# Kernel optimization log

Measured on AMD Instinct MI355X. Metric: run time of the kernel, lower is better.

The kernel has to match this reference:

```python
import jax, jax.numpy as jnp
import numpy as np

B, S, D, H = 2, 2048, 1024, 16
DH = D // H  # 64


def setup_inputs() -> dict:
    key = jax.random.key(0)
    ks = jax.random.split(key, 10)
    inp = {
        "q": jax.random.normal(ks[0], (B, S, D), jnp.float32),
        "k": jax.random.normal(ks[1], (B, S, D), jnp.float32),
        "v": jax.random.normal(ks[2], (B, S, D), jnp.float32),
        "mask": jax.random.randint(ks[3], (B, S), 0, 2, jnp.int32),
        "Wq": jax.random.normal(ks[4], (D, D), jnp.float32) * 0.02,
        "bq": jnp.zeros((D,), jnp.float32),
        "Wk": jax.random.normal(ks[5], (D, D), jnp.float32) * 0.02,
        "bk": jnp.zeros((D,), jnp.float32),
        "Wv": jax.random.normal(ks[6], (D, D), jnp.float32) * 0.02,
        "bv": jnp.zeros((D,), jnp.float32),
    }
    return inp


def _split_heads(x):
    # [B, S, D] -> [B, H, S, DH]
    b, s, _ = x.shape
    return x.reshape(b, s, H, DH).transpose(0, 2, 1, 3)


def reference(q, k, v, mask, Wq, bq, Wk, bk, Wv, bv):
    qh = _split_heads(q @ Wq + bq)
    kh = _split_heads(k @ Wk + bk)
    vh = _split_heads(v @ Wv + bv)
    # NOTE: original scales by sqrt(hidden_size), not sqrt(head_dim)
    scores = jnp.einsum("bhqd,bhkd->bhqk", qh, kh) / jnp.sqrt(jnp.float32(D))
    m = mask.astype(jnp.float32)[:, None, None, :]  # [B,1,1,S_k]
    scores = scores + (-1e9) * (1.0 - m)
    weights = jax.nn.softmax(scores, axis=-1)
    out = jnp.einsum("bhqk,bhkd->bhqd", weights, vh)
    # concat heads: [B,H,S,DH] -> [B,S,D]
    return out.transpose(0, 2, 1, 3).reshape(q.shape[0], -1, D)
```

## Files before the change

### kernel.cpp

```cpp
#include <hip/hip_runtime.h>


#define B_ 2
#define S_ 2048
#define D_ 1024
#define H_ 16
#define DH_ 64
#define M_ (B_*S_)

#define WT_OFF  ((size_t)3*4194304)
#define XB_OFF  (WT_OFF + (size_t)3*1048576)

typedef __attribute__((ext_vector_type(8))) short short8;
typedef __attribute__((ext_vector_type(4))) float f32x4;
#define MFMA16(a,b,c) __builtin_amdgcn_mfma_f32_16x16x32_bf16(a,b,c,0,0,0)

typedef __attribute__((address_space(1))) const void* gptr_t;
typedef __attribute__((address_space(3))) void* lptr_t;
static __device__ inline void gload_lds16(const void* g, void* l) {
    __builtin_amdgcn_global_load_lds((gptr_t)g, (lptr_t)l, 16, 0, 0);
}

static __device__ inline unsigned short f2bf(float x) {
    union { float f; unsigned u; } v; v.f = x;
    return (unsigned short)((v.u + 0x7fffu + ((v.u >> 16) & 1u)) >> 16);
}
static __device__ inline unsigned packp(float a, float b) {
    return __builtin_amdgcn_perm(__float_as_uint(b) + 0x8000u,
                                 __float_as_uint(a) + 0x8000u, 0x07060302u);
}

__global__ __launch_bounds__(256) void convert_x3(
    const float* __restrict__ X0, const float* __restrict__ X1,
    const float* __restrict__ X2, unsigned short* __restrict__ O0,
    unsigned short* __restrict__ O1, unsigned short* __restrict__ O2)
{
    const int z = blockIdx.z;
    const float* X = z==0 ? X0 : (z==1 ? X1 : X2);
    unsigned short* O = z==0 ? O0 : (z==1 ? O1 : O2);
    int idx = blockIdx.x*256 + threadIdx.x;
    float4 xv = *(const float4*)&X[(size_t)idx*4];
    uint2 o;
    o.x = (unsigned)f2bf(xv.x) | ((unsigned)f2bf(xv.y) << 16);
    o.y = (unsigned)f2bf(xv.z) | ((unsigned)f2bf(xv.w) << 16);
    *(uint2*)&O[(size_t)idx*4] = o;
}

__global__ __launch_bounds__(256) void convert_w(
    const float* __restrict__ Wq, const float* __restrict__ Wk,
    const float* __restrict__ Wv, unsigned short* __restrict__ WtBase)
{
    const int which = blockIdx.z;
    const float* W = which==0 ? Wq : (which==1 ? Wk : Wv);
    unsigned short* Out = WtBase + ((size_t)which << 20);

    __shared__ unsigned short T[64][72];
    const int t  = threadIdx.x;
    const int n0 = blockIdx.x*64, k0 = blockIdx.y*64;
    const int tk = t >> 4, tn4 = (t & 15)*4;

    #pragma unroll
    for (int i=0;i<4;i++){
        int kk = tk + i*16;
        float4 wv = *(const float4*)&W[(size_t)(k0+kk)*D_ + n0 + tn4];
        T[tn4+0][kk] = f2bf(wv.x);
        T[tn4+1][kk] = f2bf(wv.y);
        T[tn4+2][kk] = f2bf(wv.z);
        T[tn4+3][kk] = f2bf(wv.w);
    }
    __syncthreads();

    const int n = t >> 2, seg = t & 3;
    uint4 a = *(uint4*)&T[n][seg*16];
    uint4 b = *(uint4*)&T[n][seg*16 + 8];
    *(uint4*)&Out[(size_t)(n0+n)*D_ + k0 + seg*16]     = a;
    *(uint4*)&Out[(size_t)(n0+n)*D_ + k0 + seg*16 + 8] = b;
}

__global__ __launch_bounds__(256) void proj_gemm(
    const unsigned short* __restrict__ A0, const unsigned short* __restrict__ A1,
    const unsigned short* __restrict__ A2, const unsigned short* __restrict__ WtBase,
    const float* __restrict__ b0, const float* __restrict__ b1,
    const float* __restrict__ b2, unsigned short* __restrict__ OutBase)
{
    const int which = blockIdx.z;
    const unsigned short* A  = which==0 ? A0 : (which==1 ? A1 : A2);
    const unsigned short* Bm = WtBase + ((size_t)which << 20);
    const float* bias        = which==0 ? b0 : (which==1 ? b1 : b2);
    unsigned short* Out      = OutBase + ((size_t)which << 22);
    const float oscale = (which==0) ? 0.04508422f : 1.0f;

    __shared__ __align__(16) unsigned short As[128*64];
    __shared__ __align__(16) unsigned short Bs[128*64];

    const int t    = threadIdx.x;
    const int m0   = blockIdx.y * 128;
    const int n0   = blockIdx.x * 128;
    const int w    = t >> 6;
    const int lane = t & 63;
    const int l15  = lane & 15;
    const int quad = lane >> 4;
    const int wm   = w >> 1, wn = w & 1;

    f32x4 acc[4][4];
    #pragma unroll
    for (int i=0;i<4;i++)
        #pragma unroll
        for (int j=0;j<4;j++) acc[i][j] = (f32x4){0.f,0.f,0.f,0.f};

    float biasv[4];
    #pragma unroll
    for (int nt=0; nt<4; nt++)
        biasv[nt] = bias[n0 + wn*64 + nt*16 + l15];

    int sArow[4], sAkc[4];
    #pragma unroll
    for (int i=0;i<4;i++){
        int s  = (w*4 + i)*64 + lane;
        int r  = s >> 3, cs = s & 7;
        sArow[i] = r;
        sAkc[i]  = ((cs ^ (r & 7)) * 8);
    }

    for (int ks = 0; ks < 16; ++ks) {
        const int kb = ks * 64;
        #pragma unroll
        for (int i=0;i<4;i++){
            int s = (w*4 + i)*64 + lane;
            gload_lds16(A  + (size_t)(m0 + sArow[i])*D_ + kb + sAkc[i], (unsigned short*)As + s*8);
            gload_lds16(Bm + (size_t)(n0 + sArow[i])*D_ + kb + sAkc[i], (unsigned short*)Bs + s*8);
        }
        __syncthreads();

        #pragma unroll
        for (int kh=0; kh<2; kh++){
            short8 aF[4], bF[4];
            #pragma unroll
            for (int mt=0; mt<4; mt++){
                int r  = wm*64 + mt*16 + l15;
                int cs = (kh*4 + quad) ^ (r & 7);
                aF[mt] = *(const short8*)(As + r*64 + cs*8);
            }
            #pragma unroll
            for (int nt=0; nt<4; nt++){
                int r  = wn*64 + nt*16 + l15;
                int cs = (kh*4 + quad) ^ (r & 7);
                bF[nt] = *(const short8*)(Bs + r*64 + cs*8);
            }
            #pragma unroll
            for (int mt=0; mt<4; mt++)
                #pragma unroll
                for (int nt=0; nt<4; nt++)
                    acc[mt][nt] = MFMA16(aF[mt], bF[nt], acc[mt][nt]);
        }
        __syncthreads();
    }

    if (which != 2) {
        #pragma unroll
        for (int nt=0; nt<4; nt++){
            int n  = n0 + wn*64 + nt*16 + l15;
            int hh = n >> 6, dh = n & 63;
            #pragma unroll
            for (int mt=0; mt<4; mt++){
                #pragma unroll
                for (int r=0; r<4; r++){
                    int m  = m0 + wm*64 + mt*16 + quad*4 + r;
                    int bb = m >> 11, ss = m & (S_-1);
                    float v = (acc[mt][nt][r] + biasv[nt]) * oscale;
                    Out[((size_t)((bb*H_ + hh)*S_ + ss))*DH_ + dh] = f2bf(v);
                }
            }
        }
    } else {
        #pragma unroll
        for (int nt=0; nt<4; nt++){
            int n  = n0 + wn*64 + nt*16 + l15;
            int hh = n >> 6, dh = n & 63;
            #pragma unroll
            for (int mt=0; mt<4; mt++){
                int m  = m0 + wm*64 + mt*16 + quad*4;
                int bb = m >> 11, ss = m & (S_-1);
                uint2 pk;
                pk.x = packp(acc[mt][nt][0] + biasv[nt], acc[mt][nt][1] + biasv[nt]);
                pk.y = packp(acc[mt][nt][2] + biasv[nt], acc[mt][nt][3] + biasv[nt]);
                *(uint2*)&Out[((size_t)((bb*H_ + hh)*DH_ + dh))*S_ + ss] = pk;
            }
        }
    }
}

__global__ __launch_bounds__(256) void attn_kernel(
    const unsigned short* __restrict__ ws, const int* __restrict__ mask,
    float* __restrict__ out)
{
    const unsigned short* Qh = ws;
    const unsigned short* Kh = ws + (size_t)M_*D_;
    const unsigned short* Vg = ws + 2*(size_t)M_*D_;

    const int qt = blockIdx.x;
    const int h  = blockIdx.y;
    const int bb = blockIdx.z;
    const size_t base = ((size_t)(bb*H_ + h)) * S_ * DH_;
    const int q0 = qt * 128;

    __shared__ __align__(16) unsigned char smem[51712];
    unsigned short* KsB = (unsigned short*)smem;
    unsigned short* VtB = (unsigned short*)(smem + 16384);
    unsigned short* Pb  = (unsigned short*)(smem + 32768);
    float*          MsB = (float*)(smem + 51200);
    float*          Ob  = (float*)smem;

    const int t    = threadIdx.x;
    const int w    = t >> 6;
    const int lane = t & 63;
    const int l15  = lane & 15;
    const int quad = lane >> 4;

    short8 qf[2][2];
    #pragma unroll
    for (int qs=0; qs<2; qs++){
        const unsigned short* qp = Qh + base + (size_t)(q0 + w*32 + qs*16 + l15)*DH_ + quad*8;
        qf[qs][0] = *(const short8*)(qp);
        qf[qs][1] = *(const short8*)(qp + 32);
    }

    f32x4 accO[2][4];
    #pragma unroll
    for (int qs=0; qs<2; qs++)
        #pragma unroll
        for (int i=0;i<4;i++) accO[qs][i] = (f32x4){0.f,0.f,0.f,0.f};
    float l_run[2] = {0.f, 0.f};

    int rr[2], cc[2], ssl[2];
    #pragma unroll
    for (int i=0;i<2;i++){
        int s = (w*2 + i)*64 + lane;
        ssl[i] = s;
        rr[i]  = s >> 3;
        cc[i]  = ((s & 7) ^ (rr[i] & 7)) * 8;
    }

    #define ISSUE(k0v, p) do {                                                 \
        _Pragma("unroll")                                                      \
        for (int i=0;i<2;i++){                                                 \
            gload_lds16(Kh + base + (size_t)((k0v) + rr[i])*DH_ + cc[i],       \
                        KsB + (p)*4096 + ssl[i]*8);                            \
            gload_lds16(Vg + base + (size_t)rr[i]*S_ + (k0v) + cc[i],          \
                        VtB + (p)*4096 + ssl[i]*8);                            \
        }                                                                      \
    } while(0)

    ISSUE(0, 0);
    if (t < 64) MsB[t] = mask[bb*S_ + t] ? 0.f : -1e9f;
    __syncthreads();

    for (int it = 0; it < 32; ++it){
        const int p = it & 1;
        int mR = 0;
        if (it < 31){
            ISSUE((it+1)*64, 1-p);
            if (t < 64) mR = mask[bb*S_ + (it+1)*64 + t];
        }
        const unsigned short* Ks  = KsB + p*4096;
        const unsigned short* Vts = VtB + p*4096;
        const float* Ms = MsB + p*64;

        f32x4 msv[4];
        #pragma unroll
        for (int st=0; st<4; st++)
            msv[st] = *(const f32x4*)&Ms[st*16 + quad*4];

        f32x4 sc[2][4];
        #pragma unroll
        for (int st=0; st<4; st++){
            int key = st*16 + l15;
            const unsigned short* kr = Ks + key*64;
            short8 ka = *(const short8*)(kr + ((quad    ) ^ (key & 7))*8);
            short8 kb = *(const short8*)(kr + ((quad + 4) ^ (key & 7))*8);
            #pragma unroll
            for (int qs=0; qs<2; qs++){
                f32x4 a = (f32x4){0.f,0.f,0.f,0.f};
                a = MFMA16(ka, qf[qs][0], a);
                a = MFMA16(kb, qf[qs][1], a);
                sc[qs][st] = a;
            }
        }

        #pragma unroll
        for (int qs=0; qs<2; qs++){
            float lacc = 0.f;
            unsigned short* pr = Pb + (w*32 + qs*16 + l15)*72;
            #pragma unroll
            for (int st=0; st<4; st++){
                float pv[4];
                #pragma unroll
                for (int r=0; r<4; r++){
                    pv[r] = __builtin_amdgcn_exp2f(sc[qs][st][r] + msv[st][r]);
                    lacc += pv[r];
                }
                uint2 pk;
                pk.x = packp(pv[0], pv[1]);
                pk.y = packp(pv[2], pv[3]);
                *(uint2*)(pr + st*16 + quad*4) = pk;
            }
            l_run[qs] += lacc;
        }

        short8 vf[4][2];
        #pragma unroll
        for (int mt=0; mt<4; mt++){
            int row = mt*16 + l15;
            const unsigned short* vr = Vts + row*64;
            vf[mt][0] = *(const short8*)(vr + ((quad    ) ^ (row & 7))*8);
            vf[mt][1] = *(const short8*)(vr + ((quad + 4) ^ (row & 7))*8);
        }
        #pragma unroll
        for (int qs=0; qs<2; qs++){
            const unsigned short* pr = Pb + (w*32 + qs*16 + l15)*72;
            short8 pf0 = *(const short8*)(pr + quad*8);
            short8 pf1 = *(const short8*)(pr + 32 + quad*8);
            #pragma unroll
            for (int mt=0; mt<4; mt++){
                accO[qs][mt] = MFMA16(vf[mt][0], pf0, accO[qs][mt]);
                accO[qs][mt] = MFMA16(vf[mt][1], pf1, accO[qs][mt]);
            }
        }

        if (it < 31 && t < 64) MsB[(1-p)*64 + t] = mR ? 0.f : -1e9f;
        __syncthreads();
    }

    #pragma unroll
    for (int qs=0; qs<2; qs++){
        float l = l_run[qs];
        l += __shfl_xor(l, 16);
        l += __shfl_xor(l, 32);
        float invl = 1.0f / fmaxf(l, 1e-30f);
        #pragma unroll
        for (int mt=0; mt<4; mt++)
            #pragma unroll
            for (int r=0; r<4; r++)
                Ob[(w*32 + qs*16 + l15)*68 + mt*16 + quad*4 + r] = accO[qs][mt][r]*invl;
    }
    __syncthreads();

    #pragma unroll
    for (int i=0;i<8;i++){
        int f  = (i*256 + t)*4;
        int qq = f >> 6, dh = f & 63;
        float4 o = *(float4*)&Ob[qq*68 + dh];
        *(float4*)&out[((size_t)(bb*S_ + q0 + qq))*D_ + h*DH_ + dh] = o;
    }
    #undef ISSUE
}

extern "C" void kernel_launch(void* const* d_in, const int* in_sizes, int n_in,
                              void* d_out, int out_size, void* d_ws, size_t ws_size,
                              hipStream_t stream) {
    const float* q    = (const float*)d_in[0];
    const float* k    = (const float*)d_in[1];
    const float* v    = (const float*)d_in[2];
    const int*   mask = (const int*)d_in[3];
    const float* Wq   = (const float*)d_in[4];
    const float* b0   = (const float*)d_in[5];
    const float* Wk   = (const float*)d_in[6];
    const float* b1   = (const float*)d_in[7];
    const float* Wv   = (const float*)d_in[8];
    const float* b2   = (const float*)d_in[9];
    float* out = (float*)d_out;
    unsigned short* ws = (unsigned short*)d_ws;

    unsigned short* xq = ws + XB_OFF;
    unsigned short* xk = (unsigned short*)d_out;
    unsigned short* xv = (unsigned short*)d_out + 4194304;

    convert_w<<<dim3(16,16,3), 256, 0, stream>>>(Wq, Wk, Wv, ws + WT_OFF);
    convert_x3<<<dim3(4096,1,3), 256, 0, stream>>>(q, k, v, xq, xk, xv);
    proj_gemm<<<dim3(8,32,3), 256, 0, stream>>>(xq, xk, xv, ws + WT_OFF,
                                                b0, b1, b2, ws);
    attn_kernel<<<dim3(16,16,2), 256, 0, stream>>>(ws, mask, out);
}
```

Measured before the change: 215.5 us.

## Keep P in registers, enlarge attention query tile, merge conversion kernels

The attention kernel now builds P fragments directly in registers: it permutes the K row load order so the score MFMA output layout matches the PV MFMA input layout, which removes the LDS round trip for P. Each block now handles 256 queries (64 per wave) to reuse each K/V tile more, launches half as many blocks with a remapped block order, and writes the output in two halves through the staging buffer. The x and W bf16 conversion kernels are merged into one launch to save a launch. This raises register pressure (launch_bounds 256,1) and uses fewer blocks, which may lower occupancy and CU coverage.

```diff
diff --git a/kernel.cpp b/kernel.cpp
--- a/kernel.cpp
+++ b/kernel.cpp
@@ -13,6 +13,7 @@
 
 typedef __attribute__((ext_vector_type(8))) short short8;
 typedef __attribute__((ext_vector_type(4))) float f32x4;
+typedef __attribute__((ext_vector_type(4))) unsigned int u32x4;
 #define MFMA16(a,b,c) __builtin_amdgcn_mfma_f32_16x16x32_bf16(a,b,c,0,0,0)
 
 typedef __attribute__((address_space(1))) const void* gptr_t;
@@ -30,33 +31,34 @@
                                  __float_as_uint(a) + 0x8000u, 0x07060302u);
 }
 
-__global__ __launch_bounds__(256) void convert_x3(
+__global__ __launch_bounds__(256) void convert_all(
     const float* __restrict__ X0, const float* __restrict__ X1,
-    const float* __restrict__ X2, unsigned short* __restrict__ O0,
-    unsigned short* __restrict__ O1, unsigned short* __restrict__ O2)
+    const float* __restrict__ X2,
+    const float* __restrict__ Wq, const float* __restrict__ Wk,
+    const float* __restrict__ Wv,
+    unsigned short* __restrict__ O0, unsigned short* __restrict__ O1,
+    unsigned short* __restrict__ O2, unsigned short* __restrict__ WtBase)
 {
+    __shared__ unsigned short T[64][72];
     const int z = blockIdx.z;
-    const float* X = z==0 ? X0 : (z==1 ? X1 : X2);
-    unsigned short* O = z==0 ? O0 : (z==1 ? O1 : O2);
-    int idx = blockIdx.x*256 + threadIdx.x;
-    float4 xv = *(const float4*)&X[(size_t)idx*4];
-    uint2 o;
-    o.x = (unsigned)f2bf(xv.x) | ((unsigned)f2bf(xv.y) << 16);
-    o.y = (unsigned)f2bf(xv.z) | ((unsigned)f2bf(xv.w) << 16);
-    *(uint2*)&O[(size_t)idx*4] = o;
-}
-
-__global__ __launch_bounds__(256) void convert_w(
-    const float* __restrict__ Wq, const float* __restrict__ Wk,
-    const float* __restrict__ Wv, unsigned short* __restrict__ WtBase)
-{
-    const int which = blockIdx.z;
-    const float* W = which==0 ? Wq : (which==1 ? Wk : Wv);
-    unsigned short* Out = WtBase + ((size_t)which << 20);
-
-    __shared__ unsigned short T[64][72];
-    const int t  = threadIdx.x;
-    const int n0 = blockIdx.x*64, k0 = blockIdx.y*64;
+    const int t = threadIdx.x;
+
+    if (blockIdx.x < 4096) {
+        const float* X = z==0 ? X0 : (z==1 ? X1 : X2);
+        unsigned short* O = z==0 ? O0 : (z==1 ? O1 : O2);
+        int idx = blockIdx.x*256 + t;
+        float4 xv = *(const float4*)&X[(size_t)idx*4];
+        uint2 o;
+        o.x = (unsigned)f2bf(xv.x) | ((unsigned)f2bf(xv.y) << 16);
+        o.y = (unsigned)f2bf(xv.z) | ((unsigned)f2bf(xv.w) << 16);
+        *(uint2*)&O[(size_t)idx*4] = o;
+        return;
+    }
+
+    const float* W = z==0 ? Wq : (z==1 ? Wk : Wv);
+    unsigned short* Out = WtBase + ((size_t)z << 20);
+    const int bx2 = blockIdx.x - 4096;
+    const int n0 = (bx2 & 15)*64, k0 = (bx2 >> 4)*64;
     const int tk = t >> 4, tn4 = (t & 15)*4;
 
     #pragma unroll
@@ -190,7 +192,7 @@
     }
 }
 
-__global__ __launch_bounds__(256) void attn_kernel(
+__global__ __launch_bounds__(256, 1) void attn_kernel(
     const unsigned short* __restrict__ ws, const int* __restrict__ mask,
     float* __restrict__ out)
 {
@@ -198,17 +200,19 @@
     const unsigned short* Kh = ws + (size_t)M_*D_;
     const unsigned short* Vg = ws + 2*(size_t)M_*D_;
 
-    const int qt = blockIdx.x;
-    const int h  = blockIdx.y;
-    const int bb = blockIdx.z;
+    const int lin = blockIdx.x + (blockIdx.y << 3) + (blockIdx.z << 7);
+    const int Wn  = (lin & 7)*32 + (lin >> 3);
+    const int qt = Wn & 7;
+    const int h  = (Wn >> 3) & 15;
+    const int bb = Wn >> 7;
+
     const size_t base = ((size_t)(bb*H_ + h)) * S_ * DH_;
-    const int q0 = qt * 128;
-
-    __shared__ __align__(16) unsigned char smem[51712];
+    const int q0 = qt * 256;
+
+    __shared__ __align__(16) unsigned char smem[34816];
     unsigned short* KsB = (unsigned short*)smem;
     unsigned short* VtB = (unsigned short*)(smem + 16384);
-    unsigned short* Pb  = (unsigned short*)(smem + 32768);
-    float*          MsB = (float*)(smem + 51200);
+    float*          MsB = (float*)(smem + 32768);
     float*          Ob  = (float*)smem;
 
     const int t    = threadIdx.x;
@@ -217,34 +221,36 @@
     const int l15  = lane & 15;
     const int quad = lane >> 4;
 
-    short8 qf[2][2];
-    #pragma unroll
-    for (int qs=0; qs<2; qs++){
-        const unsigned short* qp = Qh + base + (size_t)(q0 + w*32 + qs*16 + l15)*DH_ + quad*8;
+    short8 qf[4][2];
+    #pragma unroll
+    for (int qs=0; qs<4; qs++){
+        const unsigned short* qp = Qh + base + (size_t)(q0 + w*64 + qs*16 + l15)*DH_ + quad*8;
         qf[qs][0] = *(const short8*)(qp);
         qf[qs][1] = *(const short8*)(qp + 32);
     }
 
-    f32x4 accO[2][4];
-    #pragma unroll
-    for (int qs=0; qs<2; qs++)
+    f32x4 accO[4][4];
+    #pragma unroll
+    for (int qs=0; qs<4; qs++)
         #pragma unroll
         for (int i=0;i<4;i++) accO[qs][i] = (f32x4){0.f,0.f,0.f,0.f};
-    float l_run[2] = {0.f, 0.f};
-
-    int rr[2], cc[2], ssl[2];
+    float l_run[4] = {0.f, 0.f, 0.f, 0.f};
+
+    int rr[2], cc[2], ssl[2], gK[2];
     #pragma unroll
     for (int i=0;i<2;i++){
         int s = (w*2 + i)*64 + lane;
+        int r = s >> 3, cs = s & 7;
         ssl[i] = s;
-        rr[i]  = s >> 3;
-        cc[i]  = ((s & 7) ^ (rr[i] & 7)) * 8;
+        rr[i]  = r;
+        cc[i]  = (cs ^ (r & 7)) * 8;
+        gK[i]  = ((r >> 4) & 1)*32 + ((r >> 2) & 3)*8 + (r >> 5)*4 + (r & 3);
     }
 
     #define ISSUE(k0v, p) do {                                                 \
         _Pragma("unroll")                                                      \
         for (int i=0;i<2;i++){                                                 \
-            gload_lds16(Kh + base + (size_t)((k0v) + rr[i])*DH_ + cc[i],       \
+            gload_lds16(Kh + base + (size_t)((k0v) + gK[i])*DH_ + cc[i],       \
                         KsB + (p)*4096 + ssl[i]*8);                            \
             gload_lds16(Vg + base + (size_t)rr[i]*S_ + (k0v) + cc[i],          \
                         VtB + (p)*4096 + ssl[i]*8);                            \
@@ -269,44 +275,16 @@
         f32x4 msv[4];
         #pragma unroll
         for (int st=0; st<4; st++)
-            msv[st] = *(const f32x4*)&Ms[st*16 + quad*4];
-
-        f32x4 sc[2][4];
+            msv[st] = *(const f32x4*)&Ms[(st&1)*32 + (st>>1)*4 + quad*8];
+
+        short8 ka[4], kb[4];
         #pragma unroll
         for (int st=0; st<4; st++){
-            int key = st*16 + l15;
-            const unsigned short* kr = Ks + key*64;
-            short8 ka = *(const short8*)(kr + ((quad    ) ^ (key & 7))*8);
-            short8 kb = *(const short8*)(kr + ((quad + 4) ^ (key & 7))*8);
-            #pragma unroll
-            for (int qs=0; qs<2; qs++){
-                f32x4 a = (f32x4){0.f,0.f,0.f,0.f};
-                a = MFMA16(ka, qf[qs][0], a);
-                a = MFMA16(kb, qf[qs][1], a);
-                sc[qs][st] = a;
-            }
-        }
-
-        #pragma unroll
-        for (int qs=0; qs<2; qs++){
-            float lacc = 0.f;
-            unsigned short* pr = Pb + (w*32 + qs*16 + l15)*72;
-            #pragma unroll
-            for (int st=0; st<4; st++){
-                float pv[4];
-                #pragma unroll
-                for (int r=0; r<4; r++){
-                    pv[r] = __builtin_amdgcn_exp2f(sc[qs][st][r] + msv[st][r]);
-                    lacc += pv[r];
-                }
-                uint2 pk;
-                pk.x = packp(pv[0], pv[1]);
-                pk.y = packp(pv[2], pv[3]);
-                *(uint2*)(pr + st*16 + quad*4) = pk;
-            }
-            l_run[qs] += lacc;
-        }
-
+            int row = st*16 + l15;
+            const unsigned short* kr = Ks + row*64;
+            ka[st] = *(const short8*)(kr + ((quad    ) ^ (row & 7))*8);
+            kb[st] = *(const short8*)(kr + ((quad + 4) ^ (row & 7))*8);
+        }
         short8 vf[4][2];
         #pragma unroll
         for (int mt=0; mt<4; mt++){
@@ -315,11 +293,32 @@
             vf[mt][0] = *(const short8*)(vr + ((quad    ) ^ (row & 7))*8);
             vf[mt][1] = *(const short8*)(vr + ((quad + 4) ^ (row & 7))*8);
         }
-        #pragma unroll
-        for (int qs=0; qs<2; qs++){
-            const unsigned short* pr = Pb + (w*32 + qs*16 + l15)*72;
-            short8 pf0 = *(const short8*)(pr + quad*8);
-            short8 pf1 = *(const short8*)(pr + 32 + quad*8);
+
+        #pragma unroll
+        for (int qs=0; qs<4; qs++){
+            f32x4 sc[4];
+            #pragma unroll
+            for (int st=0; st<4; st++){
+                f32x4 a = (f32x4){0.f,0.f,0.f,0.f};
+                a = MFMA16(ka[st], qf[qs][0], a);
+                a = MFMA16(kb[st], qf[qs][1], a);
+                sc[st] = a;
+            }
+            float pv[4][4]; float lacc = 0.f;
+            #pragma unroll
+            for (int st=0; st<4; st++)
+                #pragma unroll
+                for (int rj=0; rj<4; rj++){
+                    pv[st][rj] = __builtin_amdgcn_exp2f(sc[st][rj] + msv[st][rj]);
+                    lacc += pv[st][rj];
+                }
+            l_run[qs] += lacc;
+            u32x4 u0 = { packp(pv[0][0],pv[0][1]), packp(pv[0][2],pv[0][3]),
+                         packp(pv[2][0],pv[2][1]), packp(pv[2][2],pv[2][3]) };
+            u32x4 u1 = { packp(pv[1][0],pv[1][1]), packp(pv[1][2],pv[1][3]),
+                         packp(pv[3][0],pv[3][1]), packp(pv[3][2],pv[3][3]) };
+            short8 pf0 = __builtin_bit_cast(short8, u0);
+            short8 pf1 = __builtin_bit_cast(short8, u1);
             #pragma unroll
             for (int mt=0; mt<4; mt++){
                 accO[qs][mt] = MFMA16(vf[mt][0], pf0, accO[qs][mt]);
@@ -331,26 +330,35 @@
         __syncthreads();
     }
 
-    #pragma unroll
-    for (int qs=0; qs<2; qs++){
+    float invl[4];
+    #pragma unroll
+    for (int qs=0; qs<4; qs++){
         float l = l_run[qs];
         l += __shfl_xor(l, 16);
         l += __shfl_xor(l, 32);
-        float invl = 1.0f / fmaxf(l, 1e-30f);
-        #pragma unroll
-        for (int mt=0; mt<4; mt++)
-            #pragma unroll
-            for (int r=0; r<4; r++)
-                Ob[(w*32 + qs*16 + l15)*68 + mt*16 + quad*4 + r] = accO[qs][mt][r]*invl;
-    }
-    __syncthreads();
-
-    #pragma unroll
-    for (int i=0;i<8;i++){
-        int f  = (i*256 + t)*4;
-        int qq = f >> 6, dh = f & 63;
-        float4 o = *(float4*)&Ob[qq*68 + dh];
-        *(float4*)&out[((size_t)(bb*S_ + q0 + qq))*D_ + h*DH_ + dh] = o;
+        invl[qs] = 1.0f / fmaxf(l, 1e-30f);
+    }
+    #pragma unroll
+    for (int c=0; c<2; c++){
+        if ((w >> 1) == c){
+            #pragma unroll
+            for (int qs=0; qs<4; qs++)
+                #pragma unroll
+                for (int mt=0; mt<4; mt++)
+                    #pragma unroll
+                    for (int rj=0; rj<4; rj++)
+                        Ob[((w&1)*64 + qs*16 + l15)*68 + mt*16 + quad*4 + rj]
+                            = accO[qs][mt][rj]*invl[qs];
+        }
+        __syncthreads();
+        #pragma unroll
+        for (int i=0;i<8;i++){
+            int f  = (i*256 + t)*4;
+            int qq = f >> 6, dh = f & 63;
+            float4 o = *(float4*)&Ob[qq*68 + dh];
+            *(float4*)&out[((size_t)(bb*S_ + q0 + c*128 + qq))*D_ + h*DH_ + dh] = o;
+        }
+        __syncthreads();
     }
     #undef ISSUE
 }
@@ -375,9 +383,9 @@
     unsigned short* xk = (unsigned short*)d_out;
     unsigned short* xv = (unsigned short*)d_out + 4194304;
 
-    convert_w<<<dim3(16,16,3), 256, 0, stream>>>(Wq, Wk, Wv, ws + WT_OFF);
-    convert_x3<<<dim3(4096,1,3), 256, 0, stream>>>(q, k, v, xq, xk, xv);
+    convert_all<<<dim3(4352,1,3), 256, 0, stream>>>(q, k, v, Wq, Wk, Wv,
+                                                    xq, xk, xv, ws + WT_OFF);
     proj_gemm<<<dim3(8,32,3), 256, 0, stream>>>(xq, xk, xv, ws + WT_OFF,
                                                 b0, b1, b2, ws);
-    attn_kernel<<<dim3(16,16,2), 256, 0, stream>>>(ws, mask, out);
-}
+    attn_kernel<<<dim3(8,16,2), 256, 0, stream>>>(ws, mask, out);
+}
```

After: 222.9 us. +3.4%, slower.
